# Kernel optimization log

Measured on AMD Instinct MI355X. Metric: run time of the kernel, lower is better.

Reference implementation:

```python
import jax, jax.numpy as jnp
import numpy as np

D_MODEL = 1024
SCALE = 1.0 / np.sqrt(D_MODEL)


def setup_inputs() -> dict:
    key = jax.random.key(0)
    ks = jax.random.split(key, 9)
    B, S, D = 4, 2048, D_MODEL
    std = 1.0 / np.sqrt(D)
    x = jax.random.normal(ks[0], (B, S, D), dtype=jnp.float32)
    # nn.Linear weights: [out, in]; we store transposed [in, out] for x @ W
    Wq = jax.random.uniform(ks[1], (D, D), jnp.float32, -std, std)
    bq = jax.random.uniform(ks[2], (D,), jnp.float32, -std, std)
    Wk = jax.random.uniform(ks[3], (D, D), jnp.float32, -std, std)
    bk = jax.random.uniform(ks[4], (D,), jnp.float32, -std, std)
    Wv = jax.random.uniform(ks[5], (D, D), jnp.float32, -std, std)
    bv = jax.random.uniform(ks[6], (D,), jnp.float32, -std, std)
    Wo = jax.random.uniform(ks[7], (D, D), jnp.float32, -std, std)
    bo = jax.random.uniform(ks[8], (D,), jnp.float32, -std, std)
    return {"x": x, "Wq": Wq, "bq": bq, "Wk": Wk, "bk": bk,
            "Wv": Wv, "bv": bv, "Wo": Wo, "bo": bo}


def reference(x, Wq, bq, Wk, bk, Wv, bv, Wo, bo):
    q = x @ Wq + bq                      # [B,S,D]
    k = x @ Wk + bk
    v = x @ Wv + bv
    scores = jnp.einsum('bsd,btd->bst', q, k) * SCALE  # [B,S,S]
    weights = jax.nn.softmax(scores, axis=-1)
    out = jnp.einsum('bst,btd->bsd', weights, v)       # [B,S,D]
    return out @ Wo + bo
```

## Files before the change

### kernel.cpp

```cpp
#include <hip/hip_runtime.h>
#include <hip/hip_bf16.h>
#include <cstdint>

typedef __bf16 bf16x8 __attribute__((ext_vector_type(8)));
typedef float f32x4 __attribute__((ext_vector_type(4)));

__device__ __forceinline__ float bf2f(unsigned short u) {
  union { unsigned int i; float f; } x; x.i = ((unsigned int)u) << 16; return x.f;
}
__device__ __forceinline__ unsigned short f2bf(float f) {
  __hip_bfloat16 h = __float2bfloat16(f);
  return __builtin_bit_cast(unsigned short, h);
}

__device__ __forceinline__ void gload_lds16(const void* g, void* l) {
  auto gp = reinterpret_cast<__attribute__((address_space(1))) char*>(
      reinterpret_cast<uintptr_t>(g));
  auto lp = reinterpret_cast<__attribute__((address_space(3))) char*>(
      reinterpret_cast<uintptr_t>(l));
  __builtin_amdgcn_global_load_lds(gp, lp, 16, 0, 0);
}

#define SB() __builtin_amdgcn_sched_barrier(0)
#define BAR()                         \
  do {                                \
    SB();                             \
    __builtin_amdgcn_s_barrier();     \
    SB();                             \
  } while (0)
#define LGKM0()                                          \
  do {                                                   \
    asm volatile("s_waitcnt lgkmcnt(0)" ::: "memory");   \
    SB();                                                \
  } while (0)

__device__ __forceinline__ void xcd_swz(int& bx, int& by, int& bz) {
  const int gx = gridDim.x, gy = gridDim.y;
  const int n = gx * gy * (int)gridDim.z;
  int lin = blockIdx.x + gx * (blockIdx.y + gy * blockIdx.z);
  lin = (lin & 7) * (n >> 3) + (lin >> 3);
  bx = lin % gx; lin /= gx;
  by = lin % gy; bz = lin / gy;
}

__global__ __launch_bounds__(256) void cvt_f32_to_bf16(
    const float* __restrict__ in, unsigned short* __restrict__ out, long n4) {
  long i = (long)blockIdx.x * 256 + threadIdx.x;
  if (i >= n4) return;
  const float4 v = reinterpret_cast<const float4*>(in)[i];
  ushort4 o;
  o.x = f2bf(v.x); o.y = f2bf(v.y); o.z = f2bf(v.z); o.w = f2bf(v.w);
  reinterpret_cast<ushort4*>(out)[i] = o;
}

__global__ void transpose_w4(const float* __restrict__ w0,
                             const float* __restrict__ w1,
                             const float* __restrict__ w2,
                             const float* __restrict__ w3,
                             unsigned short* __restrict__ out) {
  const int z = blockIdx.z;
  const float* in = (z == 0) ? w0 : (z == 1) ? w1 : (z == 2) ? w2 : w3;
  out += (size_t)z * 1024 * 1024;
  __shared__ float tile[32][33];
  const int c0 = blockIdx.x * 32, r0 = blockIdx.y * 32;
  tile[threadIdx.y][threadIdx.x] =
      in[(size_t)(r0 + threadIdx.y) * 1024 + c0 + threadIdx.x];
  __syncthreads();
  out[(size_t)(c0 + threadIdx.y) * 1024 + r0 + threadIdx.x] =
      f2bf(tile[threadIdx.x][threadIdx.y]);
}

__global__ void concat_bias3(const float* a, const float* b, const float* c,
                             float* o) {
  int i = blockIdx.x * 256 + threadIdx.x;
  if (i >= 3072) return;
  o[i] = (i < 1024) ? a[i] : (i < 2048 ? b[i - 1024] : c[i - 2048]);
}

#define STAGE128(gbase, ld, ldsbase, rowbase)                                 \
  {                                                                           \
    _Pragma("unroll") for (int l_ = 0; l_ < 2; ++l_) {                        \
      const int seg_ = (w << 1) + l_;                                         \
      const int r0_ = (rowbase) + (seg_ << 3);                                \
      const int gr_ = r0_ + (lane >> 3);                                      \
      const int sc_ = ((lane & 7) ^ (lane >> 3)) << 3;                        \
      gload_lds16((gbase) + (size_t)gr_ * (ld) + sc_, (ldsbase) + r0_ * 64);  \
    }                                                                         \
  }

#define LDA_FRAG(dst, tile, rbase)                                            \
  _Pragma("unroll") for (int m_ = 0; m_ < 4; ++m_)                            \
  _Pragma("unroll") for (int kk_ = 0; kk_ < 2; ++kk_) {                       \
    const int row_ = (rbase) + (m_ << 4) + (lane & 15);                       \
    const int ch_ = ((kk_ << 2) + (lane >> 4)) ^ (lane & 7);                  \
    dst[m_][kk_] =                                                            \
        *reinterpret_cast<const bf16x8*>((tile) + row_ * 64 + (ch_ << 3));    \
  }
#define LDB_FRAG(dst, tile, rbase)                                            \
  _Pragma("unroll") for (int n_ = 0; n_ < 2; ++n_)                            \
  _Pragma("unroll") for (int kk_ = 0; kk_ < 2; ++kk_) {                       \
    const int row_ = (rbase) + (n_ << 4) + (lane & 15);                       \
    const int ch_ = ((kk_ << 2) + (lane >> 4)) ^ (lane & 7);                  \
    dst[n_][kk_] =                                                            \
        *reinterpret_cast<const bf16x8*>((tile) + row_ * 64 + (ch_ << 3));    \
  }

#define STAGE_A(gbase, ld, ldsbase, h)                                        \
  {                                                                           \
    _Pragma("unroll") for (int l_ = 0; l_ < 2; ++l_) {                        \
      const int seg_ = (w << 1) + l_;                                         \
      const int r0_ = ((seg_ >> 3) << 7) + ((h) << 6) + ((seg_ & 7) << 3);    \
      const int gr_ = r0_ + (lane >> 3);                                      \
      const int sc_ = ((lane & 7) ^ (lane >> 3)) << 3;                        \
      gload_lds16((gbase) + (size_t)gr_ * (ld) + sc_, (ldsbase) + r0_ * 64);  \
    }                                                                         \
  }
#define STAGE_B(gbase, ld, ldsbase, h)                                        \
  {                                                                           \
    _Pragma("unroll") for (int l_ = 0; l_ < 2; ++l_) {                        \
      const int seg_ = (w << 1) + l_;                                         \
      const int r0_ = ((seg_ >> 2) << 6) + ((h) << 5) + ((seg_ & 3) << 3);    \
      const int gr_ = r0_ + (lane >> 3);                                      \
      const int sc_ = ((lane & 7) ^ (lane >> 3)) << 3;                        \
      gload_lds16((gbase) + (size_t)gr_ * (ld) + sc_, (ldsbase) + r0_ * 64);  \
    }                                                                         \
  }

#define MFMA_QUAD(a_, b_, af_, bf_)                                           \
  __builtin_amdgcn_s_setprio(1);                                              \
  _Pragma("unroll") for (int m_ = 0; m_ < 4; ++m_)                            \
  _Pragma("unroll") for (int n_ = 0; n_ < 2; ++n_)                            \
  _Pragma("unroll") for (int kk_ = 0; kk_ < 2; ++kk_)                         \
      acc[(a_) * 4 + m_][(b_) * 2 + n_] =                                     \
          __builtin_amdgcn_mfma_f32_16x16x32_bf16(                            \
              af_[m_][kk_], bf_[n_][kk_], acc[(a_) * 4 + m_][(b_) * 2 + n_],  \
              0, 0, 0);                                                       \
  __builtin_amdgcn_s_setprio(0);

template <typename OutT, bool HAS_BIAS>
__global__ __launch_bounds__(512, 2) void gemm256(
    const unsigned short* __restrict__ A,
    const unsigned short* __restrict__ Bt,
    OutT* __restrict__ C,
    const float* __restrict__ bias,
    int K, int lda, int ldb, int ldc, float scale,
    long sA, long sB, long sC) {
  int bx, by, bz;
  xcd_swz(bx, by, bz);
  A  += (long)bz * sA;
  Bt += (long)bz * sB;
  C  += (long)bz * sC;
  const int n0 = bx << 8;
  const int m0 = by << 8;
  __shared__ __attribute__((aligned(16))) unsigned short lds[2 * 32768];
  const int t = threadIdx.x;
  const int lane = t & 63;
  const int w = t >> 6;
  const int wm = w >> 2, wn = w & 3;
  const unsigned short* gA = A + (size_t)m0 * lda;
  const unsigned short* gB = Bt + (size_t)n0 * ldb;
  const int NT = K >> 6;

  f32x4 acc[8][4];
  const f32x4 vz = {0.f, 0.f, 0.f, 0.f};
#pragma unroll
  for (int i = 0; i < 8; ++i)
#pragma unroll
    for (int j = 0; j < 4; ++j) acc[i][j] = vz;

  {
    unsigned short* a0 = lds;
    unsigned short* b0t = lds + 16384;
    STAGE_A(gA, lda, a0, 0);
    STAGE_B(gB, ldb, b0t, 0);
    STAGE_B(gB, ldb, b0t, 1);
    STAGE_A(gA, lda, a0, 1);
    if (NT > 1) {
      unsigned short* a1 = lds + 32768;
      unsigned short* b1t = lds + 32768 + 16384;
      STAGE_A(gA + 64, lda, a1, 0);
      STAGE_B(gB + 64, ldb, b1t, 0);
      STAGE_B(gB + 64, ldb, b1t, 1);
      asm volatile("s_waitcnt vmcnt(6)" ::: "memory");
    } else {
      asm volatile("s_waitcnt vmcnt(0)" ::: "memory");
    }
  }
  BAR();

  for (int kt = 0; kt < NT; ++kt) {
    unsigned short* at = lds + ((kt & 1) << 15);
    unsigned short* bt = at + 16384;
    unsigned short* atN = lds + (((kt + 1) & 1) << 15);
    const unsigned short* gA1 = gA + (size_t)(kt + 1) * 64;
    const unsigned short* gA2 = gA + (size_t)(kt + 2) * 64;
    const unsigned short* gB2 = gB + (size_t)(kt + 2) * 64;
    const bool st1 = kt + 1 < NT, st2 = kt + 2 < NT;

    bf16x8 af[4][2], b0[2][2], b1[2][2];

    LDA_FRAG(af, at, (wm << 7));
    LDB_FRAG(b0, bt, (wn << 6));
    if (st1) STAGE_A(gA1, lda, atN, 1);
    BAR();
    LGKM0();
    MFMA_QUAD(0, 0, af, b0);
    BAR();

    LDB_FRAG(b1, bt, (wn << 6) + 32);
    if (st2) STAGE_A(gA2, lda, at, 0);
    BAR();
    LGKM0();
    MFMA_QUAD(0, 1, af, b1);
    BAR();

    LDA_FRAG(af, at, (wm << 7) + 64);
    if (st2) STAGE_B(gB2, ldb, bt, 0);
    BAR();
    LGKM0();
    MFMA_QUAD(1, 0, af, b0);
    BAR();

    if (st2) STAGE_B(gB2, ldb, bt, 1);
    if (kt < NT - 3) {
      asm volatile("s_waitcnt vmcnt(6)" ::: "memory");
    } else {
      asm volatile("s_waitcnt vmcnt(0)" ::: "memory");
    }
    BAR();
    MFMA_QUAD(1, 1, af, b1);
    BAR();
  }

  const int crow0 = m0 + (wm << 7) + ((lane >> 4) << 2);
  const int ccol0 = n0 + (wn << 6) + (lane & 15);
#pragma unroll
  for (int mf = 0; mf < 8; ++mf) {
#pragma unroll
    for (int nf = 0; nf < 4; ++nf) {
      const int col = ccol0 + (nf << 4);
      const float bb = HAS_BIAS ? bias[col] : 0.f;
#pragma unroll
      for (int i = 0; i < 4; ++i) {
        const int row = crow0 + (mf << 4) + i;
        const float v = acc[mf][nf][i] * scale + bb;
        if constexpr (sizeof(OutT) == 2) {
          C[(size_t)row * ldc + col] = (OutT)f2bf(v);
        } else {
          C[(size_t)row * ldc + col] = (OutT)v;
        }
      }
    }
  }
}

#define MFMA_QUAD128(b_, af_, bf_)                                            \
  __builtin_amdgcn_s_setprio(1);                                              \
  _Pragma("unroll") for (int m_ = 0; m_ < 4; ++m_)                            \
  _Pragma("unroll") for (int n_ = 0; n_ < 2; ++n_)                            \
  _Pragma("unroll") for (int kk_ = 0; kk_ < 2; ++kk_)                         \
      acc[m_][(b_) * 2 + n_] = __builtin_amdgcn_mfma_f32_16x16x32_bf16(       \
          af_[m_][kk_], bf_[n_][kk_], acc[m_][(b_) * 2 + n_], 0, 0, 0);       \
  __builtin_amdgcn_s_setprio(0);

template <typename OutT, bool HAS_BIAS, bool VSPLIT>
__global__ __launch_bounds__(512, 2) void gemm128(
    const unsigned short* __restrict__ A,
    const unsigned short* __restrict__ Bt,
    OutT* __restrict__ C,
    const float* __restrict__ bias,
    unsigned short* __restrict__ vt,
    int K, int lda, int ldb, int ldc, float scale,
    long sA, long sB, long sC) {
  int bx, by, bz;
  xcd_swz(bx, by, bz);
  A  += (long)bz * sA;
  Bt += (long)bz * sB;
  C  += (long)bz * sC;
  const int n0 = bx << 7;
  const int m0 = by << 8;
  __shared__ __attribute__((aligned(16))) unsigned short lds[2 * 24576];
  const int t = threadIdx.x;
  const int lane = t & 63;
  const int w = t >> 6;
  const int wm = w >> 1, wn = w & 1;
  const unsigned short* gA = A + (size_t)m0 * lda;
  const unsigned short* gB = Bt + (size_t)n0 * ldb;
  const int NT = K >> 6;

  f32x4 acc[4][4];
  const f32x4 vz = {0.f, 0.f, 0.f, 0.f};
#pragma unroll
  for (int i = 0; i < 4; ++i)
#pragma unroll
    for (int j = 0; j < 4; ++j) acc[i][j] = vz;

  {
    unsigned short* a0 = lds;
    unsigned short* b0 = lds + 16384;
    STAGE128(gA, lda, a0, 0);
    STAGE128(gA, lda, a0, 128);
    STAGE128(gB, ldb, b0, 0);
    if (NT > 1) {
      unsigned short* a1 = lds + 24576;
      STAGE128(gA + 64, lda, a1, 0);
      STAGE128(gA + 64, lda, a1, 128);
      asm volatile("s_waitcnt vmcnt(4)" ::: "memory");
    } else {
      asm volatile("s_waitcnt vmcnt(0)" ::: "memory");
    }
  }
  BAR();

  for (int kt = 0; kt < NT; ++kt) {
    const int p = kt & 1;
    unsigned short* at = lds + p * 24576;
    unsigned short* btile = at + 16384;
    unsigned short* atO = lds + (p ^ 1) * 24576;
    const unsigned short* gB1 = gB + (size_t)(kt + 1) * 64;
    const unsigned short* gA2 = gA + (size_t)(kt + 2) * 64;
    const bool st1 = kt + 1 < NT, st2 = kt + 2 < NT;

    bf16x8 af[4][2], b0[2][2], b1[2][2];

    LDA_FRAG(af, at, (wm << 6));
    LDB_FRAG(b0, btile, (wn << 6));
    if (st1) STAGE128(gB1, ldb, atO + 16384, 0);
    BAR();
    LGKM0();
    MFMA_QUAD128(0, af, b0);
    BAR();

    LDB_FRAG(b1, btile, (wn << 6) + 32);
    if (st2) {
      STAGE128(gA2, lda, at, 0);
      STAGE128(gA2, lda, at, 128);
    }
    if (kt < NT - 2) {
      asm volatile("s_waitcnt vmcnt(4)" ::: "memory");
    } else {
      asm volatile("s_waitcnt vmcnt(0)" ::: "memory");
    }
    BAR();
    LGKM0();
    MFMA_QUAD128(1, af, b1);
    BAR();
  }

  const int crow0 = m0 + (wm << 6) + ((lane >> 4) << 2);
  const int ccol0 = n0 + (wn << 6) + (lane & 15);

  if (VSPLIT && n0 >= 2048) {
    const int b = m0 >> 11;
#pragma unroll
    for (int mf = 0; mf < 4; ++mf) {
#pragma unroll
      for (int nf = 0; nf < 4; ++nf) {
        const int col = ccol0 + (nf << 4);
        const float bb = HAS_BIAS ? bias[col] : 0.f;
        const int d = col - 2048;
        const int s = (crow0 & 2047) + (mf << 4);
        ushort4 o;
        o.x = f2bf(acc[mf][nf][0] * scale + bb);
        o.y = f2bf(acc[mf][nf][1] * scale + bb);
        o.z = f2bf(acc[mf][nf][2] * scale + bb);
        o.w = f2bf(acc[mf][nf][3] * scale + bb);
        *reinterpret_cast<ushort4*>(vt + (((size_t)b << 10) + d) * 2048 + s) = o;
      }
    }
    return;
  }

#pragma unroll
  for (int mf = 0; mf < 4; ++mf) {
#pragma unroll
    for (int nf = 0; nf < 4; ++nf) {
      const int col = ccol0 + (nf << 4);
      const float bb = HAS_BIAS ? bias[col] : 0.f;
#pragma unroll
      for (int i = 0; i < 4; ++i) {
        const int row = crow0 + (mf << 4) + i;
        const float v = acc[mf][nf][i] * scale + bb;
        if constexpr (sizeof(OutT) == 2) {
          C[(size_t)row * ldc + col] = (OutT)f2bf(v);
        } else {
          C[(size_t)row * ldc + col] = (OutT)v;
        }
      }
    }
  }
}

__global__ __launch_bounds__(256) void softmax_inplace(
    unsigned short* __restrict__ P, int S) {
  const size_t row = blockIdx.x;
  unsigned short* p = P + row * (size_t)S;
  const int t = threadIdx.x;
  const int lane = t & 63, w = t >> 6;
  const uint4 raw = reinterpret_cast<const uint4*>(p)[t];
  unsigned int u[4] = {raw.x, raw.y, raw.z, raw.w};
  float v[8];
#pragma unroll
  for (int j = 0; j < 4; ++j) {
    v[2 * j]     = bf2f((unsigned short)(u[j] & 0xffffu));
    v[2 * j + 1] = bf2f((unsigned short)(u[j] >> 16));
  }
  float mx = v[0];
#pragma unroll
  for (int j = 1; j < 8; ++j) mx = fmaxf(mx, v[j]);
#pragma unroll
  for (int off = 32; off >= 1; off >>= 1) mx = fmaxf(mx, __shfl_xor(mx, off, 64));
  __shared__ float red[4];
  if (lane == 0) red[w] = mx;
  __syncthreads();
  mx = fmaxf(fmaxf(red[0], red[1]), fmaxf(red[2], red[3]));
  float e[8];
  float s = 0.f;
#pragma unroll
  for (int j = 0; j < 8; ++j) { e[j] = __expf(v[j] - mx); s += e[j]; }
#pragma unroll
  for (int off = 32; off >= 1; off >>= 1) s += __shfl_xor(s, off, 64);
  __syncthreads();
  if (lane == 0) red[w] = s;
  __syncthreads();
  s = red[0] + red[1] + red[2] + red[3];
  const float inv = 1.f / s;
  unsigned int o[4];
#pragma unroll
  for (int j = 0; j < 4; ++j)
    o[j] = (unsigned int)f2bf(e[2 * j] * inv) |
           ((unsigned int)f2bf(e[2 * j + 1] * inv) << 16);
  uint4 ov; ov.x = o[0]; ov.y = o[1]; ov.z = o[2]; ov.w = o[3];
  reinterpret_cast<uint4*>(p)[t] = ov;
}

extern "C" void kernel_launch(void* const* d_in, const int* in_sizes, int n_in,
                              void* d_out, int out_size, void* d_ws, size_t ws_size,
                              hipStream_t stream) {
  (void)in_sizes; (void)n_in; (void)out_size; (void)ws_size;
  const float* x  = (const float*)d_in[0];
  const float* Wq = (const float*)d_in[1];
  const float* bq = (const float*)d_in[2];
  const float* Wk = (const float*)d_in[3];
  const float* bk = (const float*)d_in[4];
  const float* Wv = (const float*)d_in[5];
  const float* bv = (const float*)d_in[6];
  const float* Wo = (const float*)d_in[7];
  const float* bo = (const float*)d_in[8];
  float* out = (float*)d_out;

  constexpr int B = 4, S = 2048, D = 1024;
  constexpr long BS = (long)B * S;
  constexpr size_t MB = 1ull << 20;
  char* ws = (char*)d_ws;
  unsigned short* xb   = (unsigned short*)(ws + 0);
  unsigned short* Wall = (unsigned short*)(ws + 16 * MB);
  float*          bqkv = (float*)(ws + 24 * MB);
  unsigned short* QKVc = (unsigned short*)(ws + 25 * MB);
  unsigned short* Vt   = (unsigned short*)(ws + 57 * MB);
  unsigned short* Sc   = (unsigned short*)(ws + 73 * MB);
  unsigned short* AO   = (unsigned short*)(ws + 0);

  const float scale = 0.03125f;

  cvt_f32_to_bf16<<<(BS * D / 4 + 255) / 256, 256, 0, stream>>>(x, xb, BS * D / 4);
  transpose_w4<<<dim3(32, 32, 4), dim3(32, 32), 0, stream>>>(Wq, Wk, Wv, Wo, Wall);
  concat_bias3<<<12, 256, 0, stream>>>(bq, bk, bv, bqkv);

  gemm128<unsigned short, true, true><<<dim3(24, 32, 1), 512, 0, stream>>>(
      xb, Wall, QKVc, bqkv, Vt, D, D, D, 2048, 1.f, 0, 0, 0);

  gemm256<unsigned short, false><<<dim3(S / 256, S / 256, B), 512, 0, stream>>>(
      QKVc + 0, QKVc + 1024, Sc, nullptr, D, 2048, 2048, S, scale,
      (long)S * 2048, (long)S * 2048, (long)S * S);

  softmax_inplace<<<B * S, 256, 0, stream>>>(Sc, S);

  gemm128<unsigned short, false, false><<<dim3(8, 8, 4), 512, 0, stream>>>(
      Sc, Vt, AO, nullptr, nullptr, S, S, S, D, 1.f,
      (long)S * S, (long)D * S, (long)S * D);

  gemm128<float, true, false><<<dim3(8, 32, 1), 512, 0, stream>>>(
      AO, Wall + 3 * 1024 * 1024, out, bo, nullptr, D, D, D, D, 1.f, 0, 0, 0);
}
```

Baseline: 204.4 us.

## Triple-buffer LDS tiles in gemm128 to prefetch two K-steps ahead

Replaces the double-buffered A/B LDS staging in the 128-wide GEMM with a three-slot ring buffer, so the A and B tiles for step kt+2 are staged while step kt computes. The aim is to hide more global-load latency behind the MFMA work in the QKV, PV and output-projection GEMMs. LDS use per block grows from 96KB to 144KB. That likely stops two 512-thread blocks from co-residing on a CU, which the launch bounds request, and so could cut occupancy.

```diff
diff --git a/kernel.cpp b/kernel.cpp
--- a/kernel.cpp
+++ b/kernel.cpp
@@ -264,7 +264,7 @@
   __builtin_amdgcn_s_setprio(0);
 
 template <typename OutT, bool HAS_BIAS, bool VSPLIT>
-__global__ __launch_bounds__(512, 2) void gemm128(
+__global__ __launch_bounds__(512, 2) void gemm128t(
     const unsigned short* __restrict__ A,
     const unsigned short* __restrict__ Bt,
     OutT* __restrict__ C,
@@ -279,7 +279,7 @@
   C  += (long)bz * sC;
   const int n0 = bx << 7;
   const int m0 = by << 8;
-  __shared__ __attribute__((aligned(16))) unsigned short lds[2 * 24576];
+  __shared__ __attribute__((aligned(16))) unsigned short lds[3 * 24576];
   const int t = threadIdx.x;
   const int lane = t & 63;
   const int w = t >> 6;
@@ -296,55 +296,52 @@
     for (int j = 0; j < 4; ++j) acc[i][j] = vz;
 
   {
-    unsigned short* a0 = lds;
-    unsigned short* b0 = lds + 16384;
-    STAGE128(gA, lda, a0, 0);
-    STAGE128(gA, lda, a0, 128);
-    STAGE128(gB, ldb, b0, 0);
-    if (NT > 1) {
-      unsigned short* a1 = lds + 24576;
-      STAGE128(gA + 64, lda, a1, 0);
-      STAGE128(gA + 64, lda, a1, 128);
-      asm volatile("s_waitcnt vmcnt(4)" ::: "memory");
+    STAGE128(gA, lda, lds, 0);
+    STAGE128(gA, lda, lds, 128);
+    STAGE128(gB, ldb, lds + 16384, 0);
+    STAGE128(gA + 64, lda, lds + 24576, 0);
+    STAGE128(gA + 64, lda, lds + 24576, 128);
+    STAGE128(gB + 64, ldb, lds + 24576 + 16384, 0);
+    asm volatile("s_waitcnt vmcnt(6)" ::: "memory");
+  }
+  BAR();
+
+  int idx = 0;
+  for (int kt = 0; kt < NT; ++kt) {
+    unsigned short* at = lds + idx * 24576;
+    unsigned short* btile = at + 16384;
+    int idx2 = idx + 2; if (idx2 >= 3) idx2 -= 3;
+    unsigned short* st = lds + idx2 * 24576;
+    const unsigned short* gA2 = gA + (size_t)(kt + 2) * 64;
+    const unsigned short* gB2 = gB + (size_t)(kt + 2) * 64;
+    const bool st2 = kt + 2 < NT;
+
+    bf16x8 af[4][2], b0[2][2], b1[2][2];
+
+    LDA_FRAG(af, at, (wm << 6));
+    LDB_FRAG(b0, btile, (wn << 6));
+    if (st2) {
+      STAGE128(gA2, lda, st, 0);
+      STAGE128(gA2, lda, st, 128);
+    }
+    BAR();
+    LGKM0();
+    MFMA_QUAD128(0, af, b0);
+    BAR();
+
+    LDB_FRAG(b1, btile, (wn << 6) + 32);
+    if (st2) STAGE128(gB2, ldb, st + 16384, 0);
+    if (kt < NT - 2) {
+      asm volatile("s_waitcnt vmcnt(6)" ::: "memory");
     } else {
       asm volatile("s_waitcnt vmcnt(0)" ::: "memory");
     }
-  }
-  BAR();
-
-  for (int kt = 0; kt < NT; ++kt) {
-    const int p = kt & 1;
-    unsigned short* at = lds + p * 24576;
-    unsigned short* btile = at + 16384;
-    unsigned short* atO = lds + (p ^ 1) * 24576;
-    const unsigned short* gB1 = gB + (size_t)(kt + 1) * 64;
-    const unsigned short* gA2 = gA + (size_t)(kt + 2) * 64;
-    const bool st1 = kt + 1 < NT, st2 = kt + 2 < NT;
-
-    bf16x8 af[4][2], b0[2][2], b1[2][2];
-
-    LDA_FRAG(af, at, (wm << 6));
-    LDB_FRAG(b0, btile, (wn << 6));
-    if (st1) STAGE128(gB1, ldb, atO + 16384, 0);
-    BAR();
-    LGKM0();
-    MFMA_QUAD128(0, af, b0);
-    BAR();
-
-    LDB_FRAG(b1, btile, (wn << 6) + 32);
-    if (st2) {
-      STAGE128(gA2, lda, at, 0);
-      STAGE128(gA2, lda, at, 128);
-    }
-    if (kt < NT - 2) {
-      asm volatile("s_waitcnt vmcnt(4)" ::: "memory");
-    } else {
-      asm volatile("s_waitcnt vmcnt(0)" ::: "memory");
-    }
     BAR();
     LGKM0();
     MFMA_QUAD128(1, af, b1);
     BAR();
+
+    idx = (idx + 1 == 3) ? 0 : idx + 1;
   }
 
   const int crow0 = m0 + (wm << 6) + ((lane >> 4) << 2);
@@ -467,7 +464,7 @@
   transpose_w4<<<dim3(32, 32, 4), dim3(32, 32), 0, stream>>>(Wq, Wk, Wv, Wo, Wall);
   concat_bias3<<<12, 256, 0, stream>>>(bq, bk, bv, bqkv);
 
-  gemm128<unsigned short, true, true><<<dim3(24, 32, 1), 512, 0, stream>>>(
+  gemm128t<unsigned short, true, true><<<dim3(24, 32, 1), 512, 0, stream>>>(
       xb, Wall, QKVc, bqkv, Vt, D, D, D, 2048, 1.f, 0, 0, 0);
 
   gemm256<unsigned short, false><<<dim3(S / 256, S / 256, B), 512, 0, stream>>>(
@@ -476,10 +473,10 @@
 
   softmax_inplace<<<B * S, 256, 0, stream>>>(Sc, S);
 
-  gemm128<unsigned short, false, false><<<dim3(8, 8, 4), 512, 0, stream>>>(
+  gemm128t<unsigned short, false, false><<<dim3(8, 8, 4), 512, 0, stream>>>(
       Sc, Vt, AO, nullptr, nullptr, S, S, S, D, 1.f,
       (long)S * S, (long)D * S, (long)S * D);
 
-  gemm128<float, true, false><<<dim3(8, 32, 1), 512, 0, stream>>>(
+  gemm128t<float, true, false><<<dim3(8, 32, 1), 512, 0, stream>>>(
       AO, Wall + 3 * 1024 * 1024, out, bo, nullptr, D, D, D, D, 1.f, 0, 0, 0);
 }
```

Result: no change. 205.1 us (+0.3%).
